# Kernel optimization log

Hardware: AMD Instinct MI355X
Metric: run time of the kernel (lower is better)

Reference implementation:

```python
import jax, jax.numpy as jnp
import numpy as np

D_IN = 2048
D_SAE = 16384
N_RANGES = 4
CTX = 128  # batch == context_length
CHUNK = D_SAE // N_RANGES
LN_EPS = 1e-5


def setup_inputs() -> dict:
    key = jax.random.key(0)
    k1, k2, k3, k4 = jax.random.split(key, 4)
    acts = jax.random.normal(k1, (CTX, D_IN), dtype=jnp.float32)
    # orthogonal-init stand-ins: unit-variance columns
    W_enc_ranges = jax.random.normal(k2, (N_RANGES, D_IN, CHUNK), dtype=jnp.float32) / np.sqrt(D_IN)
    W_dec = jax.random.normal(k3, (D_SAE, D_IN), dtype=jnp.float32) / np.sqrt(D_SAE)
    pos_embeddings = jax.random.normal(k4, (N_RANGES, D_IN), dtype=jnp.float32) * 0.02
    return {
        "acts": acts,
        "W_enc_ranges": W_enc_ranges,
        "b_enc": jnp.zeros((D_SAE,), jnp.float32),
        "b_dec": jnp.zeros((D_IN,), jnp.float32),
        "pos_embeddings": pos_embeddings,
        "ln_weight": jnp.ones((D_SAE,), jnp.float32),
        "ln_bias": jnp.zeros((D_SAE,), jnp.float32),
        "W_dec": W_dec,
    }


def reference(acts, W_enc_ranges, b_enc, b_dec, pos_embeddings, ln_weight, ln_bias, W_dec):
    B, d_in = acts.shape
    n_ranges, _, chunk = W_enc_ranges.shape
    range_size = B // n_ranges  # positions are contiguous blocks per range
    d_sae = n_ranges * chunk

    # gather per position range: [n_ranges, range_size, d_in]
    x = acts.reshape(n_ranges, range_size, d_in)
    x = x + pos_embeddings[:, None, :] - b_dec  # (input + pos_emb) - b_dec

    # per-range GEMM + bias
    pre = jnp.einsum("rbd,rds->rbs", x, W_enc_ranges) + b_enc.reshape(n_ranges, 1, chunk)

    # per-range LayerNorm over the chunk (sliced gamma/beta), biased variance
    mu = jnp.mean(pre, axis=-1, keepdims=True)
    var = jnp.mean(jnp.square(pre - mu), axis=-1, keepdims=True)
    normed = (pre - mu) * jax.lax.rsqrt(var + LN_EPS)
    normed = normed * ln_weight.reshape(n_ranges, 1, chunk) + ln_bias.reshape(n_ranges, 1, chunk)
    feat = jax.nn.relu(normed)  # [n_ranges, range_size, chunk]

    # scatter into block-diagonal encoded [B, d_sae]
    encoded = jnp.zeros((B, d_sae), acts.dtype)
    for r in range(n_ranges):
        encoded = encoded.at[r * range_size:(r + 1) * range_size,
                             r * chunk:(r + 1) * chunk].set(feat[r])

    # decode
    decoded = encoded @ W_dec + b_dec
    return decoded
```

## Files before the change

kernel.cpp:

```cpp
#include <hip/hip_runtime.h>
#include <hip/hip_bf16.h>
#include <stdint.h>


#define D_IN   2048
#define CHUNK  4096
#define RS     32
#define LN_EPS 1e-5f

typedef __attribute__((ext_vector_type(8))) short bf16x8;
typedef __attribute__((ext_vector_type(4))) float f32x4;

#define AS1 __attribute__((address_space(1)))
#define AS3 __attribute__((address_space(3)))

__device__ __forceinline__ void gload_lds16(const float* g, float* l) {
  __builtin_amdgcn_global_load_lds((const AS1 unsigned int*)g,
                                   (AS3 unsigned int*)l, 16, 0, 0);
}

__device__ __forceinline__ unsigned short f2bf(float f) {
  unsigned int u = __float_as_uint(f);
  u += 0x7fffu + ((u >> 16) & 1u);
  return (unsigned short)(u >> 16);
}
__device__ __forceinline__ float bf2f(unsigned short s) {
  return __uint_as_float(((unsigned int)s) << 16);
}

#define MFMA16 __builtin_amdgcn_mfma_f32_16x16x32_bf16

__global__ __launch_bounds__(256) void prep_kernel(
    const float* __restrict__ acts, const float* __restrict__ pos,
    const float* __restrict__ bdec, unsigned short* __restrict__ xfrag) {
  unsigned tid = blockIdx.x * 256u + threadIdx.x;
  unsigned lane = tid & 63u, kt = (tid >> 6) & 63u, mt = (tid >> 12) & 1u, r = tid >> 13;
  unsigned m  = mt * 16 + (lane & 15u);
  unsigned k0 = kt * 32 + (lane >> 4) * 8;
  const float* ap = acts + (size_t)(r * RS + m) * D_IN + k0;
  const float* pp = pos  + (size_t)r * D_IN + k0;
  const float* bp = bdec + k0;
  bf16x8 v;
#pragma unroll
  for (int j = 0; j < 8; ++j) v[j] = (short)f2bf(ap[j] + pp[j] - bp[j]);
  *reinterpret_cast<bf16x8*>(xfrag + (size_t)tid * 8) = v;
}

__global__ __launch_bounds__(256) void enc_kernel(
    const unsigned short* __restrict__ xfrag, const float* __restrict__ Wenc,
    unsigned short* __restrict__ pre_part) {
  const unsigned r = blockIdx.x >> 8, h = (blockIdx.x >> 7) & 1u, nt = blockIdx.x & 127u;
  const unsigned n0 = nt * 32;
  const unsigned w = threadIdx.x >> 6, lane = threadIdx.x & 63u;
  const unsigned col = lane & 15u, g = lane >> 4;

  __shared__ float smem[8192];
  float* mytile = smem + w * 2048;

  const unsigned srow = lane >> 3, scol = (lane & 7u) * 4u;
  const float* gbase = Wenc
      + ((size_t)(r * D_IN + h * 1024 + w * 32 + srow)) * CHUNK + n0 + scol;
  const unsigned short* xa0 = xfrag + ((size_t)(r * 2 + 0) * 64) * 512 + (size_t)lane * 8;
  const unsigned short* xa1 = xfrag + ((size_t)(r * 2 + 1) * 64) * 512 + (size_t)lane * 8;

  f32x4 acc00 = {0.f,0.f,0.f,0.f}, acc01 = acc00, acc10 = acc00, acc11 = acc00;

  auto stageW = [&](unsigned s, unsigned b) {
#pragma unroll
    for (int l = 0; l < 4; ++l) {
      const float* gp = gbase + (size_t)(s * 128 + l * 8) * CHUNK;
      gload_lds16(gp, mytile + b * 1024 + l * 256);
    }
  };

  bf16x8 aC0, aC1, aN0, aN1;
  {
    unsigned kt = h * 32 + w;
    aC0 = *(const bf16x8*)(xa0 + (size_t)kt * 512);
    aC1 = *(const bf16x8*)(xa1 + (size_t)kt * 512);
  }
  stageW(0, 0);

  unsigned buf = 0;
#pragma unroll
  for (int s = 0; s < 8; ++s) {
    if (s < 7) {
      unsigned kt = h * 32 + (s + 1) * 4 + w;
      aN0 = *(const bf16x8*)(xa0 + (size_t)kt * 512);
      aN1 = *(const bf16x8*)(xa1 + (size_t)kt * 512);
      stageW(s + 1, buf ^ 1);
      asm volatile("s_waitcnt vmcnt(6)" ::: "memory");
    } else {
      asm volatile("s_waitcnt vmcnt(0)" ::: "memory");
    }
    const float* tb = mytile + buf * 1024 + g * 8 * 32 + col;
    bf16x8 b0, b1;
#pragma unroll
    for (int j = 0; j < 8; ++j) {
      b0[j] = (short)f2bf(tb[j * 32]);
      b1[j] = (short)f2bf(tb[j * 32 + 16]);
    }
    acc00 = MFMA16(aC0, b0, acc00, 0, 0, 0);
    acc01 = MFMA16(aC0, b1, acc01, 0, 0, 0);
    acc10 = MFMA16(aC1, b0, acc10, 0, 0, 0);
    acc11 = MFMA16(aC1, b1, acc11, 0, 0, 0);
    aC0 = aN0; aC1 = aN1; buf ^= 1;
  }

  __syncthreads();
  float* red = smem;
  if (w > 0) {
#pragma unroll
    for (int i = 0; i < 4; ++i) {
      red[(((w - 1) * 4 + 0) * 64 + lane) * 4 + i] = acc00[i];
      red[(((w - 1) * 4 + 1) * 64 + lane) * 4 + i] = acc01[i];
      red[(((w - 1) * 4 + 2) * 64 + lane) * 4 + i] = acc10[i];
      red[(((w - 1) * 4 + 3) * 64 + lane) * 4 + i] = acc11[i];
    }
  }
  __syncthreads();
  if (w == 0) {
    for (int q = 0; q < 3; ++q)
#pragma unroll
      for (int i = 0; i < 4; ++i) {
        acc00[i] += red[((q * 4 + 0) * 64 + lane) * 4 + i];
        acc01[i] += red[((q * 4 + 1) * 64 + lane) * 4 + i];
        acc10[i] += red[((q * 4 + 2) * 64 + lane) * 4 + i];
        acc11[i] += red[((q * 4 + 3) * 64 + lane) * 4 + i];
      }
    unsigned short* pp = pre_part + (size_t)h * 128 * CHUNK;
#pragma unroll
    for (int i = 0; i < 4; ++i) {
      unsigned row0 = r * RS + g * 4 + i;
      unsigned row1 = row0 + 16;
      pp[(size_t)row0 * CHUNK + n0 + col]      = f2bf(acc00[i]);
      pp[(size_t)row0 * CHUNK + n0 + 16 + col] = f2bf(acc01[i]);
      pp[(size_t)row1 * CHUNK + n0 + col]      = f2bf(acc10[i]);
      pp[(size_t)row1 * CHUNK + n0 + 16 + col] = f2bf(acc11[i]);
    }
  }
}

__global__ __launch_bounds__(256) void lnpack_kernel(
    const unsigned short* __restrict__ pre_part, const float* __restrict__ benc,
    const float* __restrict__ gamma, const float* __restrict__ beta,
    unsigned short* __restrict__ featfrag) {
  const unsigned row = blockIdx.x;
  const unsigned r = row >> 5, m = row & 31u;
  const unsigned t = threadIdx.x;
  const unsigned c0 = t * 16;

  const unsigned short* p0 = pre_part + (size_t)row * CHUNK + c0;
  const unsigned short* p1 = p0 + (size_t)128 * CHUNK;
  const float* bb = benc + (size_t)r * CHUNK + c0;

  bf16x8 u0a = *(const bf16x8*)p0, u0b = *(const bf16x8*)(p0 + 8);
  bf16x8 u1a = *(const bf16x8*)p1, u1b = *(const bf16x8*)(p1 + 8);

  float v[16];
  float s = 0.f, q = 0.f;
#pragma unroll
  for (int j = 0; j < 8; ++j) {
    v[j]     = bf2f((unsigned short)u0a[j]) + bf2f((unsigned short)u1a[j]) + bb[j];
    v[j + 8] = bf2f((unsigned short)u0b[j]) + bf2f((unsigned short)u1b[j]) + bb[j + 8];
  }
#pragma unroll
  for (int j = 0; j < 16; ++j) { s += v[j]; q += v[j] * v[j]; }
#pragma unroll
  for (int off = 1; off < 64; off <<= 1) {
    s += __shfl_xor(s, off, 64);
    q += __shfl_xor(q, off, 64);
  }
  __shared__ float ls[4], lq[4];
  if ((t & 63u) == 0) { ls[t >> 6] = s; lq[t >> 6] = q; }
  __syncthreads();
  s = ls[0] + ls[1] + ls[2] + ls[3];
  q = lq[0] + lq[1] + lq[2] + lq[3];
  float mu  = s * (1.f / CHUNK);
  float var = q * (1.f / CHUNK) - mu * mu;
  float rsd = rsqrtf(var + LN_EPS);

  const float* gp = gamma + (size_t)r * CHUNK + c0;
  const float* bp = beta  + (size_t)r * CHUNK + c0;
  const unsigned mt = m >> 4;
#pragma unroll
  for (int half = 0; half < 2; ++half) {
    bf16x8 o;
#pragma unroll
    for (int j = 0; j < 8; ++j) {
      float x = (v[half * 8 + j] - mu) * rsd * gp[half * 8 + j] + bp[half * 8 + j];
      o[j] = (short)f2bf(fmaxf(x, 0.f));
    }
    unsigned k = c0 + half * 8;
    unsigned kt = k >> 5, grp = (k >> 3) & 3u, ln = (m & 15u) + 16u * grp;
    *(bf16x8*)(featfrag + (((size_t)(r * 2 + mt) * 128 + kt) * 64 + ln) * 8) = o;
  }
}

__global__ __launch_bounds__(256) void dec_kernel(
    const unsigned short* __restrict__ featfrag, const float* __restrict__ Wdec,
    float* __restrict__ part) {
  const unsigned r = blockIdx.x >> 8, h = (blockIdx.x >> 6) & 3u, nt = blockIdx.x & 63u;
  const unsigned n0 = nt * 32;
  const unsigned w = threadIdx.x >> 6, lane = threadIdx.x & 63u;
  const unsigned col = lane & 15u, g = lane >> 4;

  __shared__ float smem[8192];
  float* mytile = smem + w * 2048;

  const unsigned srow = lane >> 3, scol = (lane & 7u) * 4u;
  const float* gbase = Wdec
      + ((size_t)(r * CHUNK + h * 1024 + w * 32 + srow)) * D_IN + n0 + scol;
  const unsigned short* fa0 = featfrag + ((size_t)(r * 2 + 0) * 128) * 512 + (size_t)lane * 8;
  const unsigned short* fa1 = featfrag + ((size_t)(r * 2 + 1) * 128) * 512 + (size_t)lane * 8;

  f32x4 acc00 = {0.f,0.f,0.f,0.f}, acc01 = acc00, acc10 = acc00, acc11 = acc00;

  auto stageW = [&](unsigned s, unsigned b) {
#pragma unroll
    for (int l = 0; l < 4; ++l) {
      const float* gp = gbase + (size_t)(s * 128 + l * 8) * D_IN;
      gload_lds16(gp, mytile + b * 1024 + l * 256);
    }
  };

  bf16x8 aC0, aC1, aN0, aN1;
  {
    unsigned kt = h * 32 + w;
    aC0 = *(const bf16x8*)(fa0 + (size_t)kt * 512);
    aC1 = *(const bf16x8*)(fa1 + (size_t)kt * 512);
  }
  stageW(0, 0);

  unsigned buf = 0;
#pragma unroll
  for (int s = 0; s < 8; ++s) {
    if (s < 7) {
      unsigned kt = h * 32 + (s + 1) * 4 + w;
      aN0 = *(const bf16x8*)(fa0 + (size_t)kt * 512);
      aN1 = *(const bf16x8*)(fa1 + (size_t)kt * 512);
      stageW(s + 1, buf ^ 1);
      asm volatile("s_waitcnt vmcnt(6)" ::: "memory");
    } else {
      asm volatile("s_waitcnt vmcnt(0)" ::: "memory");
    }
    const float* tb = mytile + buf * 1024 + g * 8 * 32 + col;
    bf16x8 b0, b1;
#pragma unroll
    for (int j = 0; j < 8; ++j) {
      b0[j] = (short)f2bf(tb[j * 32]);
      b1[j] = (short)f2bf(tb[j * 32 + 16]);
    }
    acc00 = MFMA16(aC0, b0, acc00, 0, 0, 0);
    acc01 = MFMA16(aC0, b1, acc01, 0, 0, 0);
    acc10 = MFMA16(aC1, b0, acc10, 0, 0, 0);
    acc11 = MFMA16(aC1, b1, acc11, 0, 0, 0);
    aC0 = aN0; aC1 = aN1; buf ^= 1;
  }

  __syncthreads();
  float* red = smem;
  if (w > 0) {
#pragma unroll
    for (int i = 0; i < 4; ++i) {
      red[(((w - 1) * 4 + 0) * 64 + lane) * 4 + i] = acc00[i];
      red[(((w - 1) * 4 + 1) * 64 + lane) * 4 + i] = acc01[i];
      red[(((w - 1) * 4 + 2) * 64 + lane) * 4 + i] = acc10[i];
      red[(((w - 1) * 4 + 3) * 64 + lane) * 4 + i] = acc11[i];
    }
  }
  __syncthreads();
  if (w == 0) {
    for (int q = 0; q < 3; ++q)
#pragma unroll
      for (int i = 0; i < 4; ++i) {
        acc00[i] += red[((q * 4 + 0) * 64 + lane) * 4 + i];
        acc01[i] += red[((q * 4 + 1) * 64 + lane) * 4 + i];
        acc10[i] += red[((q * 4 + 2) * 64 + lane) * 4 + i];
        acc11[i] += red[((q * 4 + 3) * 64 + lane) * 4 + i];
      }
    float* pp = part + (size_t)h * 128 * D_IN;
#pragma unroll
    for (int i = 0; i < 4; ++i) {
      unsigned row0 = r * RS + g * 4 + i;
      unsigned row1 = row0 + 16;
      pp[(size_t)row0 * D_IN + n0 + col]      = acc00[i];
      pp[(size_t)row0 * D_IN + n0 + 16 + col] = acc01[i];
      pp[(size_t)row1 * D_IN + n0 + col]      = acc10[i];
      pp[(size_t)row1 * D_IN + n0 + 16 + col] = acc11[i];
    }
  }
}

__global__ __launch_bounds__(256) void finish_kernel(
    const float* __restrict__ part, const float* __restrict__ bdec,
    float* __restrict__ out) {
  unsigned i = blockIdx.x * 256u + threadIdx.x;
  const size_t stride = (size_t)128 * D_IN / 4;
  f32x4 a0 = ((const f32x4*)part)[i];
  f32x4 a1 = ((const f32x4*)part)[i + stride];
  f32x4 a2 = ((const f32x4*)part)[i + 2 * stride];
  f32x4 a3 = ((const f32x4*)part)[i + 3 * stride];
  f32x4 c  = ((const f32x4*)bdec)[i & 511u];
  f32x4 o;
#pragma unroll
  for (int j = 0; j < 4; ++j) o[j] = ((a0[j] + a1[j]) + (a2[j] + a3[j])) + c[j];
  ((f32x4*)out)[i] = o;
}

extern "C" void kernel_launch(void* const* d_in, const int* in_sizes, int n_in,
                              void* d_out, int out_size, void* d_ws, size_t ws_size,
                              hipStream_t stream) {
  const float* acts = (const float*)d_in[0];
  const float* Wenc = (const float*)d_in[1];
  const float* benc = (const float*)d_in[2];
  const float* bdec = (const float*)d_in[3];
  const float* pos  = (const float*)d_in[4];
  const float* lnw  = (const float*)d_in[5];
  const float* lnb  = (const float*)d_in[6];
  const float* Wdec = (const float*)d_in[7];
  float* out = (float*)d_out;

  char* ws = (char*)d_ws;
  unsigned short* xfrag   = (unsigned short*)ws;
  unsigned short* pre_prt = (unsigned short*)(ws + 512 * 1024);
  unsigned short* featfrg = (unsigned short*)(ws + 2560 * 1024);
  float* part             = (float*)(ws + 3584 * 1024);

  prep_kernel  <<<128,  256, 0, stream>>>(acts, pos, bdec, xfrag);
  enc_kernel   <<<1024, 256, 0, stream>>>(xfrag, Wenc, pre_prt);
  lnpack_kernel<<<128,  256, 0, stream>>>(pre_prt, benc, lnw, lnb, featfrg);
  dec_kernel   <<<1024, 256, 0, stream>>>(featfrg, Wdec, part);
  finish_kernel<<<256,  256, 0, stream>>>(part, bdec, out);
}
```

Measured before the change: 65.77 us.

## Widen GEMM N-tiles, split K across blocks, triple-buffer weight staging

Encoder and decoder GEMM blocks now cover 128 output columns with each wave owning 32 columns, instead of splitting K across waves and reducing through shared memory. K is split across 8 (encoder) or 16 (decoder) blocks, and the partial sums are written in bf16 and summed later in the LN and finish kernels. Weight tiles are loaded into a shared 3-stage ring with block barriers, aiming for wider coalesced global loads and no intra-block reduction. The cost is more partial-sum traffic and lower accuracy from bf16 partials.

```diff
diff --git a/kernel.cpp b/kernel.cpp
--- a/kernel.cpp
+++ b/kernel.cpp
@@ -9,6 +9,7 @@
 #define LN_EPS 1e-5f
 
 typedef __attribute__((ext_vector_type(8))) short bf16x8;
+typedef __attribute__((ext_vector_type(4))) short bf16x4;
 typedef __attribute__((ext_vector_type(4))) float f32x4;
 
 #define AS1 __attribute__((address_space(1)))
@@ -49,95 +50,73 @@
 __global__ __launch_bounds__(256) void enc_kernel(
     const unsigned short* __restrict__ xfrag, const float* __restrict__ Wenc,
     unsigned short* __restrict__ pre_part) {
-  const unsigned r = blockIdx.x >> 8, h = (blockIdx.x >> 7) & 1u, nt = blockIdx.x & 127u;
-  const unsigned n0 = nt * 32;
+  const unsigned r = blockIdx.x >> 8;
+  const unsigned h = (blockIdx.x >> 5) & 7u;
+  const unsigned nt = blockIdx.x & 31u;
+  const unsigned n0 = nt * 128;
   const unsigned w = threadIdx.x >> 6, lane = threadIdx.x & 63u;
   const unsigned col = lane & 15u, g = lane >> 4;
 
-  __shared__ float smem[8192];
-  float* mytile = smem + w * 2048;
-
-  const unsigned srow = lane >> 3, scol = (lane & 7u) * 4u;
-  const float* gbase = Wenc
-      + ((size_t)(r * D_IN + h * 1024 + w * 32 + srow)) * CHUNK + n0 + scol;
+  __shared__ float tiles[3][32 * 128];
+
+  const unsigned srow = w * 8 + (lane >> 5);
+  const unsigned scol = (lane & 31u) * 4u;
+  const float* gbase = Wenc + ((size_t)(r * D_IN + h * 256 + srow)) * CHUNK + n0 + scol;
   const unsigned short* xa0 = xfrag + ((size_t)(r * 2 + 0) * 64) * 512 + (size_t)lane * 8;
   const unsigned short* xa1 = xfrag + ((size_t)(r * 2 + 1) * 64) * 512 + (size_t)lane * 8;
 
   f32x4 acc00 = {0.f,0.f,0.f,0.f}, acc01 = acc00, acc10 = acc00, acc11 = acc00;
 
-  auto stageW = [&](unsigned s, unsigned b) {
+  auto stageW = [&](int s, int b) {
 #pragma unroll
     for (int l = 0; l < 4; ++l) {
-      const float* gp = gbase + (size_t)(s * 128 + l * 8) * CHUNK;
-      gload_lds16(gp, mytile + b * 1024 + l * 256);
-    }
+      const float* gp = gbase + (size_t)(s * 32 + 2 * l) * CHUNK;
+      gload_lds16(gp, &tiles[b][(w * 8 + 2 * l) * 128]);
+    }
+  };
+  auto loadA = [&](int s, bf16x8& A0, bf16x8& A1) {
+    unsigned kt = h * 8 + (unsigned)s;
+    A0 = *(const bf16x8*)(xa0 + (size_t)kt * 512);
+    A1 = *(const bf16x8*)(xa1 + (size_t)kt * 512);
   };
 
   bf16x8 aC0, aC1, aN0, aN1;
-  {
-    unsigned kt = h * 32 + w;
-    aC0 = *(const bf16x8*)(xa0 + (size_t)kt * 512);
-    aC1 = *(const bf16x8*)(xa1 + (size_t)kt * 512);
-  }
   stageW(0, 0);
-
-  unsigned buf = 0;
+  loadA(0, aC0, aC1);
+  stageW(1, 1);
+
 #pragma unroll
   for (int s = 0; s < 8; ++s) {
-    if (s < 7) {
-      unsigned kt = h * 32 + (s + 1) * 4 + w;
-      aN0 = *(const bf16x8*)(xa0 + (size_t)kt * 512);
-      aN1 = *(const bf16x8*)(xa1 + (size_t)kt * 512);
-      stageW(s + 1, buf ^ 1);
-      asm volatile("s_waitcnt vmcnt(6)" ::: "memory");
-    } else {
-      asm volatile("s_waitcnt vmcnt(0)" ::: "memory");
-    }
-    const float* tb = mytile + buf * 1024 + g * 8 * 32 + col;
+    if (s < 7) asm volatile("s_waitcnt vmcnt(4)" ::: "memory");
+    else       asm volatile("s_waitcnt vmcnt(0)" ::: "memory");
+    __builtin_amdgcn_s_barrier();
+    __builtin_amdgcn_sched_barrier(0);
+    if (s < 7) loadA(s + 1, aN0, aN1);
+    if (s < 6) stageW(s + 2, (s + 2) % 3);
+    const float* tb = &tiles[s % 3][(g * 8) * 128 + w * 32 + col];
     bf16x8 b0, b1;
 #pragma unroll
     for (int j = 0; j < 8; ++j) {
-      b0[j] = (short)f2bf(tb[j * 32]);
-      b1[j] = (short)f2bf(tb[j * 32 + 16]);
+      b0[j] = (short)f2bf(tb[j * 128]);
+      b1[j] = (short)f2bf(tb[j * 128 + 16]);
     }
     acc00 = MFMA16(aC0, b0, acc00, 0, 0, 0);
     acc01 = MFMA16(aC0, b1, acc01, 0, 0, 0);
     acc10 = MFMA16(aC1, b0, acc10, 0, 0, 0);
     acc11 = MFMA16(aC1, b1, acc11, 0, 0, 0);
-    aC0 = aN0; aC1 = aN1; buf ^= 1;
-  }
-
-  __syncthreads();
-  float* red = smem;
-  if (w > 0) {
-#pragma unroll
-    for (int i = 0; i < 4; ++i) {
-      red[(((w - 1) * 4 + 0) * 64 + lane) * 4 + i] = acc00[i];
-      red[(((w - 1) * 4 + 1) * 64 + lane) * 4 + i] = acc01[i];
-      red[(((w - 1) * 4 + 2) * 64 + lane) * 4 + i] = acc10[i];
-      red[(((w - 1) * 4 + 3) * 64 + lane) * 4 + i] = acc11[i];
-    }
-  }
-  __syncthreads();
-  if (w == 0) {
-    for (int q = 0; q < 3; ++q)
-#pragma unroll
-      for (int i = 0; i < 4; ++i) {
-        acc00[i] += red[((q * 4 + 0) * 64 + lane) * 4 + i];
-        acc01[i] += red[((q * 4 + 1) * 64 + lane) * 4 + i];
-        acc10[i] += red[((q * 4 + 2) * 64 + lane) * 4 + i];
-        acc11[i] += red[((q * 4 + 3) * 64 + lane) * 4 + i];
-      }
-    unsigned short* pp = pre_part + (size_t)h * 128 * CHUNK;
-#pragma unroll
-    for (int i = 0; i < 4; ++i) {
-      unsigned row0 = r * RS + g * 4 + i;
-      unsigned row1 = row0 + 16;
-      pp[(size_t)row0 * CHUNK + n0 + col]      = f2bf(acc00[i]);
-      pp[(size_t)row0 * CHUNK + n0 + 16 + col] = f2bf(acc01[i]);
-      pp[(size_t)row1 * CHUNK + n0 + col]      = f2bf(acc10[i]);
-      pp[(size_t)row1 * CHUNK + n0 + 16 + col] = f2bf(acc11[i]);
-    }
+    aC0 = aN0; aC1 = aN1;
+  }
+
+  unsigned short* pp = pre_part + (size_t)h * 128 * CHUNK;
+  const unsigned nc = n0 + w * 32 + col;
+#pragma unroll
+  for (int i = 0; i < 4; ++i) {
+    unsigned row0 = r * RS + g * 4 + i;
+    unsigned row1 = row0 + 16;
+    pp[(size_t)row0 * CHUNK + nc]      = f2bf(acc00[i]);
+    pp[(size_t)row0 * CHUNK + nc + 16] = f2bf(acc01[i]);
+    pp[(size_t)row1 * CHUNK + nc]      = f2bf(acc10[i]);
+    pp[(size_t)row1 * CHUNK + nc + 16] = f2bf(acc11[i]);
   }
 }
 
@@ -150,20 +129,21 @@
   const unsigned t = threadIdx.x;
   const unsigned c0 = t * 16;
 
-  const unsigned short* p0 = pre_part + (size_t)row * CHUNK + c0;
-  const unsigned short* p1 = p0 + (size_t)128 * CHUNK;
   const float* bb = benc + (size_t)r * CHUNK + c0;
-
-  bf16x8 u0a = *(const bf16x8*)p0, u0b = *(const bf16x8*)(p0 + 8);
-  bf16x8 u1a = *(const bf16x8*)p1, u1b = *(const bf16x8*)(p1 + 8);
-
   float v[16];
+#pragma unroll
+  for (int j = 0; j < 16; ++j) v[j] = bb[j];
+#pragma unroll
+  for (int hh = 0; hh < 8; ++hh) {
+    const unsigned short* ph = pre_part + ((size_t)hh * 128 + row) * CHUNK + c0;
+    bf16x8 ua = *(const bf16x8*)ph, ub = *(const bf16x8*)(ph + 8);
+#pragma unroll
+    for (int j = 0; j < 8; ++j) {
+      v[j]     += bf2f((unsigned short)ua[j]);
+      v[j + 8] += bf2f((unsigned short)ub[j]);
+    }
+  }
   float s = 0.f, q = 0.f;
-#pragma unroll
-  for (int j = 0; j < 8; ++j) {
-    v[j]     = bf2f((unsigned short)u0a[j]) + bf2f((unsigned short)u1a[j]) + bb[j];
-    v[j + 8] = bf2f((unsigned short)u0b[j]) + bf2f((unsigned short)u1b[j]) + bb[j + 8];
-  }
 #pragma unroll
   for (int j = 0; j < 16; ++j) { s += v[j]; q += v[j] * v[j]; }
 #pragma unroll
@@ -199,112 +179,88 @@
 
 __global__ __launch_bounds__(256) void dec_kernel(
     const unsigned short* __restrict__ featfrag, const float* __restrict__ Wdec,
-    float* __restrict__ part) {
-  const unsigned r = blockIdx.x >> 8, h = (blockIdx.x >> 6) & 3u, nt = blockIdx.x & 63u;
-  const unsigned n0 = nt * 32;
+    unsigned short* __restrict__ part) {
+  const unsigned r = blockIdx.x >> 8;
+  const unsigned h = (blockIdx.x >> 4) & 15u;
+  const unsigned nt = blockIdx.x & 15u;
+  const unsigned n0 = nt * 128;
   const unsigned w = threadIdx.x >> 6, lane = threadIdx.x & 63u;
   const unsigned col = lane & 15u, g = lane >> 4;
 
-  __shared__ float smem[8192];
-  float* mytile = smem + w * 2048;
-
-  const unsigned srow = lane >> 3, scol = (lane & 7u) * 4u;
-  const float* gbase = Wdec
-      + ((size_t)(r * CHUNK + h * 1024 + w * 32 + srow)) * D_IN + n0 + scol;
+  __shared__ float tiles[3][32 * 128];
+
+  const unsigned srow = w * 8 + (lane >> 5);
+  const unsigned scol = (lane & 31u) * 4u;
+  const float* gbase = Wdec + ((size_t)(r * CHUNK + h * 256 + srow)) * D_IN + n0 + scol;
   const unsigned short* fa0 = featfrag + ((size_t)(r * 2 + 0) * 128) * 512 + (size_t)lane * 8;
   const unsigned short* fa1 = featfrag + ((size_t)(r * 2 + 1) * 128) * 512 + (size_t)lane * 8;
 
   f32x4 acc00 = {0.f,0.f,0.f,0.f}, acc01 = acc00, acc10 = acc00, acc11 = acc00;
 
-  auto stageW = [&](unsigned s, unsigned b) {
+  auto stageW = [&](int s, int b) {
 #pragma unroll
     for (int l = 0; l < 4; ++l) {
-      const float* gp = gbase + (size_t)(s * 128 + l * 8) * D_IN;
-      gload_lds16(gp, mytile + b * 1024 + l * 256);
-    }
+      const float* gp = gbase + (size_t)(s * 32 + 2 * l) * D_IN;
+      gload_lds16(gp, &tiles[b][(w * 8 + 2 * l) * 128]);
+    }
+  };
+  auto loadA = [&](int s, bf16x8& A0, bf16x8& A1) {
+    unsigned kt = h * 8 + (unsigned)s;
+    A0 = *(const bf16x8*)(fa0 + (size_t)kt * 512);
+    A1 = *(const bf16x8*)(fa1 + (size_t)kt * 512);
   };
 
   bf16x8 aC0, aC1, aN0, aN1;
-  {
-    unsigned kt = h * 32 + w;
-    aC0 = *(const bf16x8*)(fa0 + (size_t)kt * 512);
-    aC1 = *(const bf16x8*)(fa1 + (size_t)kt * 512);
-  }
   stageW(0, 0);
-
-  unsigned buf = 0;
+  loadA(0, aC0, aC1);
+  stageW(1, 1);
+
 #pragma unroll
   for (int s = 0; s < 8; ++s) {
-    if (s < 7) {
-      unsigned kt = h * 32 + (s + 1) * 4 + w;
-      aN0 = *(const bf16x8*)(fa0 + (size_t)kt * 512);
-      aN1 = *(const bf16x8*)(fa1 + (size_t)kt * 512);
-      stageW(s + 1, buf ^ 1);
-      asm volatile("s_waitcnt vmcnt(6)" ::: "memory");
-    } else {
-      asm volatile("s_waitcnt vmcnt(0)" ::: "memory");
-    }
-    const float* tb = mytile + buf * 1024 + g * 8 * 32 + col;
+    if (s < 7) asm volatile("s_waitcnt vmcnt(4)" ::: "memory");
+    else       asm volatile("s_waitcnt vmcnt(0)" ::: "memory");
+    __builtin_amdgcn_s_barrier();
+    __builtin_amdgcn_sched_barrier(0);
+    if (s < 7) loadA(s + 1, aN0, aN1);
+    if (s < 6) stageW(s + 2, (s + 2) % 3);
+    const float* tb = &tiles[s % 3][(g * 8) * 128 + w * 32 + col];
     bf16x8 b0, b1;
 #pragma unroll
     for (int j = 0; j < 8; ++j) {
-      b0[j] = (short)f2bf(tb[j * 32]);
-      b1[j] = (short)f2bf(tb[j * 32 + 16]);
+      b0[j] = (short)f2bf(tb[j * 128]);
+      b1[j] = (short)f2bf(tb[j * 128 + 16]);
     }
     acc00 = MFMA16(aC0, b0, acc00, 0, 0, 0);
     acc01 = MFMA16(aC0, b1, acc01, 0, 0, 0);
     acc10 = MFMA16(aC1, b0, acc10, 0, 0, 0);
     acc11 = MFMA16(aC1, b1, acc11, 0, 0, 0);
-    aC0 = aN0; aC1 = aN1; buf ^= 1;
-  }
-
-  __syncthreads();
-  float* red = smem;
-  if (w > 0) {
-#pragma unroll
-    for (int i = 0; i < 4; ++i) {
-      red[(((w - 1) * 4 + 0) * 64 + lane) * 4 + i] = acc00[i];
-      red[(((w - 1) * 4 + 1) * 64 + lane) * 4 + i] = acc01[i];
-      red[(((w - 1) * 4 + 2) * 64 + lane) * 4 + i] = acc10[i];
-      red[(((w - 1) * 4 + 3) * 64 + lane) * 4 + i] = acc11[i];
-    }
-  }
-  __syncthreads();
-  if (w == 0) {
-    for (int q = 0; q < 3; ++q)
-#pragma unroll
-      for (int i = 0; i < 4; ++i) {
-        acc00[i] += red[((q * 4 + 0) * 64 + lane) * 4 + i];
-        acc01[i] += red[((q * 4 + 1) * 64 + lane) * 4 + i];
-        acc10[i] += red[((q * 4 + 2) * 64 + lane) * 4 + i];
-        acc11[i] += red[((q * 4 + 3) * 64 + lane) * 4 + i];
-      }
-    float* pp = part + (size_t)h * 128 * D_IN;
-#pragma unroll
-    for (int i = 0; i < 4; ++i) {
-      unsigned row0 = r * RS + g * 4 + i;
-      unsigned row1 = row0 + 16;
-      pp[(size_t)row0 * D_IN + n0 + col]      = acc00[i];
-      pp[(size_t)row0 * D_IN + n0 + 16 + col] = acc01[i];
-      pp[(size_t)row1 * D_IN + n0 + col]      = acc10[i];
-      pp[(size_t)row1 * D_IN + n0 + 16 + col] = acc11[i];
-    }
+    aC0 = aN0; aC1 = aN1;
+  }
+
+  unsigned short* pp = part + (size_t)h * 128 * D_IN;
+  const unsigned nc = n0 + w * 32 + col;
+#pragma unroll
+  for (int i = 0; i < 4; ++i) {
+    unsigned row0 = r * RS + g * 4 + i;
+    unsigned row1 = row0 + 16;
+    pp[(size_t)row0 * D_IN + nc]      = f2bf(acc00[i]);
+    pp[(size_t)row0 * D_IN + nc + 16] = f2bf(acc01[i]);
+    pp[(size_t)row1 * D_IN + nc]      = f2bf(acc10[i]);
+    pp[(size_t)row1 * D_IN + nc + 16] = f2bf(acc11[i]);
   }
 }
 
 __global__ __launch_bounds__(256) void finish_kernel(
-    const float* __restrict__ part, const float* __restrict__ bdec,
+    const unsigned short* __restrict__ part, const float* __restrict__ bdec,
     float* __restrict__ out) {
   unsigned i = blockIdx.x * 256u + threadIdx.x;
-  const size_t stride = (size_t)128 * D_IN / 4;
-  f32x4 a0 = ((const f32x4*)part)[i];
-  f32x4 a1 = ((const f32x4*)part)[i + stride];
-  f32x4 a2 = ((const f32x4*)part)[i + 2 * stride];
-  f32x4 a3 = ((const f32x4*)part)[i + 3 * stride];
-  f32x4 c  = ((const f32x4*)bdec)[i & 511u];
-  f32x4 o;
-#pragma unroll
-  for (int j = 0; j < 4; ++j) o[j] = ((a0[j] + a1[j]) + (a2[j] + a3[j])) + c[j];
+  f32x4 o = ((const f32x4*)bdec)[i & 511u];
+#pragma unroll
+  for (int hh = 0; hh < 16; ++hh) {
+    bf16x4 u = *(const bf16x4*)(part + (size_t)hh * 128 * D_IN + (size_t)i * 4);
+#pragma unroll
+    for (int j = 0; j < 4; ++j) o[j] += bf2f((unsigned short)u[j]);
+  }
   ((f32x4*)out)[i] = o;
 }
 
@@ -324,8 +280,8 @@
   char* ws = (char*)d_ws;
   unsigned short* xfrag   = (unsigned short*)ws;
   unsigned short* pre_prt = (unsigned short*)(ws + 512 * 1024);
-  unsigned short* featfrg = (unsigned short*)(ws + 2560 * 1024);
-  float* part             = (float*)(ws + 3584 * 1024);
+  unsigned short* featfrg = (unsigned short*)(ws + 512 * 1024 + 8*1024*1024);
+  unsigned short* part    = (unsigned short*)(ws + 512 * 1024 + 9*1024*1024);
 
   prep_kernel  <<<128,  256, 0, stream>>>(acts, pos, bdec, xfrag);
   enc_kernel   <<<1024, 256, 0, stream>>>(xfrag, Wenc, pre_prt);
```

Measured after the change: 69.56 us. 5.8% more time.

## Remove split-K partials in encoder and decoder, fuse bias into decoder

Applied to the files above, without the earlier changes.

The encoder no longer splits K into two halves, so each block covers the full 2048 reduction and the LayerNorm kernel reads a single pre-activation buffer instead of summing two partials. The decoder drops its 4-way K split by using 512-thread blocks with 8 waves over the full chunk. It adds b_dec and writes the output directly, which removes the finish kernel and the fp32 partial buffer round-trip. Cost: grid sizes fall to 512 and 256 blocks, so fewer blocks are in flight to stream the weights on a GPU with many CUs, and each block runs a longer serial loop.

```diff
diff --git a/kernel.cpp b/kernel.cpp
--- a/kernel.cpp
+++ b/kernel.cpp
@@ -48,8 +48,8 @@
 
 __global__ __launch_bounds__(256) void enc_kernel(
     const unsigned short* __restrict__ xfrag, const float* __restrict__ Wenc,
-    unsigned short* __restrict__ pre_part) {
-  const unsigned r = blockIdx.x >> 8, h = (blockIdx.x >> 7) & 1u, nt = blockIdx.x & 127u;
+    unsigned short* __restrict__ pre) {
+  const unsigned r = blockIdx.x >> 7, nt = blockIdx.x & 127u;
   const unsigned n0 = nt * 32;
   const unsigned w = threadIdx.x >> 6, lane = threadIdx.x & 63u;
   const unsigned col = lane & 15u, g = lane >> 4;
@@ -59,7 +59,7 @@
 
   const unsigned srow = lane >> 3, scol = (lane & 7u) * 4u;
   const float* gbase = Wenc
-      + ((size_t)(r * D_IN + h * 1024 + w * 32 + srow)) * CHUNK + n0 + scol;
+      + ((size_t)(r * D_IN + w * 32 + srow)) * CHUNK + n0 + scol;
   const unsigned short* xa0 = xfrag + ((size_t)(r * 2 + 0) * 64) * 512 + (size_t)lane * 8;
   const unsigned short* xa1 = xfrag + ((size_t)(r * 2 + 1) * 64) * 512 + (size_t)lane * 8;
 
@@ -75,7 +75,7 @@
 
   bf16x8 aC0, aC1, aN0, aN1;
   {
-    unsigned kt = h * 32 + w;
+    unsigned kt = w;
     aC0 = *(const bf16x8*)(xa0 + (size_t)kt * 512);
     aC1 = *(const bf16x8*)(xa1 + (size_t)kt * 512);
   }
@@ -83,9 +83,9 @@
 
   unsigned buf = 0;
 #pragma unroll
-  for (int s = 0; s < 8; ++s) {
-    if (s < 7) {
-      unsigned kt = h * 32 + (s + 1) * 4 + w;
+  for (int s = 0; s < 16; ++s) {
+    if (s < 15) {
+      unsigned kt = (s + 1) * 4 + w;
       aN0 = *(const bf16x8*)(xa0 + (size_t)kt * 512);
       aN1 = *(const bf16x8*)(xa1 + (size_t)kt * 512);
       stageW(s + 1, buf ^ 1);
@@ -128,21 +128,20 @@
         acc10[i] += red[((q * 4 + 2) * 64 + lane) * 4 + i];
         acc11[i] += red[((q * 4 + 3) * 64 + lane) * 4 + i];
       }
-    unsigned short* pp = pre_part + (size_t)h * 128 * CHUNK;
 #pragma unroll
     for (int i = 0; i < 4; ++i) {
       unsigned row0 = r * RS + g * 4 + i;
       unsigned row1 = row0 + 16;
-      pp[(size_t)row0 * CHUNK + n0 + col]      = f2bf(acc00[i]);
-      pp[(size_t)row0 * CHUNK + n0 + 16 + col] = f2bf(acc01[i]);
-      pp[(size_t)row1 * CHUNK + n0 + col]      = f2bf(acc10[i]);
-      pp[(size_t)row1 * CHUNK + n0 + 16 + col] = f2bf(acc11[i]);
+      pre[(size_t)row0 * CHUNK + n0 + col]      = f2bf(acc00[i]);
+      pre[(size_t)row0 * CHUNK + n0 + 16 + col] = f2bf(acc01[i]);
+      pre[(size_t)row1 * CHUNK + n0 + col]      = f2bf(acc10[i]);
+      pre[(size_t)row1 * CHUNK + n0 + 16 + col] = f2bf(acc11[i]);
     }
   }
 }
 
 __global__ __launch_bounds__(256) void lnpack_kernel(
-    const unsigned short* __restrict__ pre_part, const float* __restrict__ benc,
+    const unsigned short* __restrict__ pre, const float* __restrict__ benc,
     const float* __restrict__ gamma, const float* __restrict__ beta,
     unsigned short* __restrict__ featfrag) {
   const unsigned row = blockIdx.x;
@@ -150,19 +149,17 @@
   const unsigned t = threadIdx.x;
   const unsigned c0 = t * 16;
 
-  const unsigned short* p0 = pre_part + (size_t)row * CHUNK + c0;
-  const unsigned short* p1 = p0 + (size_t)128 * CHUNK;
+  const unsigned short* p0 = pre + (size_t)row * CHUNK + c0;
   const float* bb = benc + (size_t)r * CHUNK + c0;
 
-  bf16x8 u0a = *(const bf16x8*)p0, u0b = *(const bf16x8*)(p0 + 8);
-  bf16x8 u1a = *(const bf16x8*)p1, u1b = *(const bf16x8*)(p1 + 8);
+  bf16x8 ua = *(const bf16x8*)p0, ub = *(const bf16x8*)(p0 + 8);
 
   float v[16];
   float s = 0.f, q = 0.f;
 #pragma unroll
   for (int j = 0; j < 8; ++j) {
-    v[j]     = bf2f((unsigned short)u0a[j]) + bf2f((unsigned short)u1a[j]) + bb[j];
-    v[j + 8] = bf2f((unsigned short)u0b[j]) + bf2f((unsigned short)u1b[j]) + bb[j + 8];
+    v[j]     = bf2f((unsigned short)ua[j]) + bb[j];
+    v[j + 8] = bf2f((unsigned short)ub[j]) + bb[j + 8];
   }
 #pragma unroll
   for (int j = 0; j < 16; ++j) { s += v[j]; q += v[j] * v[j]; }
@@ -197,20 +194,20 @@
   }
 }
 
-__global__ __launch_bounds__(256) void dec_kernel(
+__global__ __launch_bounds__(512) void dec_kernel(
     const unsigned short* __restrict__ featfrag, const float* __restrict__ Wdec,
-    float* __restrict__ part) {
-  const unsigned r = blockIdx.x >> 8, h = (blockIdx.x >> 6) & 3u, nt = blockIdx.x & 63u;
+    const float* __restrict__ bdec, float* __restrict__ out) {
+  const unsigned r = blockIdx.x >> 6, nt = blockIdx.x & 63u;
   const unsigned n0 = nt * 32;
   const unsigned w = threadIdx.x >> 6, lane = threadIdx.x & 63u;
   const unsigned col = lane & 15u, g = lane >> 4;
 
-  __shared__ float smem[8192];
+  __shared__ float smem[16384];
   float* mytile = smem + w * 2048;
 
   const unsigned srow = lane >> 3, scol = (lane & 7u) * 4u;
   const float* gbase = Wdec
-      + ((size_t)(r * CHUNK + h * 1024 + w * 32 + srow)) * D_IN + n0 + scol;
+      + ((size_t)(r * CHUNK + w * 32 + srow)) * D_IN + n0 + scol;
   const unsigned short* fa0 = featfrag + ((size_t)(r * 2 + 0) * 128) * 512 + (size_t)lane * 8;
   const unsigned short* fa1 = featfrag + ((size_t)(r * 2 + 1) * 128) * 512 + (size_t)lane * 8;
 
@@ -219,14 +216,14 @@
   auto stageW = [&](unsigned s, unsigned b) {
 #pragma unroll
     for (int l = 0; l < 4; ++l) {
-      const float* gp = gbase + (size_t)(s * 128 + l * 8) * D_IN;
+      const float* gp = gbase + (size_t)(s * 256 + l * 8) * D_IN;
       gload_lds16(gp, mytile + b * 1024 + l * 256);
     }
   };
 
   bf16x8 aC0, aC1, aN0, aN1;
   {
-    unsigned kt = h * 32 + w;
+    unsigned kt = w;
     aC0 = *(const bf16x8*)(fa0 + (size_t)kt * 512);
     aC1 = *(const bf16x8*)(fa1 + (size_t)kt * 512);
   }
@@ -234,9 +231,9 @@
 
   unsigned buf = 0;
 #pragma unroll
-  for (int s = 0; s < 8; ++s) {
-    if (s < 7) {
-      unsigned kt = h * 32 + (s + 1) * 4 + w;
+  for (int s = 0; s < 16; ++s) {
+    if (s < 15) {
+      unsigned kt = (s + 1) * 8 + w;
       aN0 = *(const bf16x8*)(fa0 + (size_t)kt * 512);
       aN1 = *(const bf16x8*)(fa1 + (size_t)kt * 512);
       stageW(s + 1, buf ^ 1);
@@ -271,7 +268,7 @@
   }
   __syncthreads();
   if (w == 0) {
-    for (int q = 0; q < 3; ++q)
+    for (int q = 0; q < 7; ++q)
 #pragma unroll
       for (int i = 0; i < 4; ++i) {
         acc00[i] += red[((q * 4 + 0) * 64 + lane) * 4 + i];
@@ -279,33 +276,17 @@
         acc10[i] += red[((q * 4 + 2) * 64 + lane) * 4 + i];
         acc11[i] += red[((q * 4 + 3) * 64 + lane) * 4 + i];
       }
-    float* pp = part + (size_t)h * 128 * D_IN;
+    float b0 = bdec[n0 + col], b1 = bdec[n0 + 16 + col];
 #pragma unroll
     for (int i = 0; i < 4; ++i) {
       unsigned row0 = r * RS + g * 4 + i;
       unsigned row1 = row0 + 16;
-      pp[(size_t)row0 * D_IN + n0 + col]      = acc00[i];
-      pp[(size_t)row0 * D_IN + n0 + 16 + col] = acc01[i];
-      pp[(size_t)row1 * D_IN + n0 + col]      = acc10[i];
-      pp[(size_t)row1 * D_IN + n0 + 16 + col] = acc11[i];
-    }
-  }
-}
-
-__global__ __launch_bounds__(256) void finish_kernel(
-    const float* __restrict__ part, const float* __restrict__ bdec,
-    float* __restrict__ out) {
-  unsigned i = blockIdx.x * 256u + threadIdx.x;
-  const size_t stride = (size_t)128 * D_IN / 4;
-  f32x4 a0 = ((const f32x4*)part)[i];
-  f32x4 a1 = ((const f32x4*)part)[i + stride];
-  f32x4 a2 = ((const f32x4*)part)[i + 2 * stride];
-  f32x4 a3 = ((const f32x4*)part)[i + 3 * stride];
-  f32x4 c  = ((const f32x4*)bdec)[i & 511u];
-  f32x4 o;
-#pragma unroll
-  for (int j = 0; j < 4; ++j) o[j] = ((a0[j] + a1[j]) + (a2[j] + a3[j])) + c[j];
-  ((f32x4*)out)[i] = o;
+      out[(size_t)row0 * D_IN + n0 + col]      = acc00[i] + b0;
+      out[(size_t)row0 * D_IN + n0 + 16 + col] = acc01[i] + b1;
+      out[(size_t)row1 * D_IN + n0 + col]      = acc10[i] + b0;
+      out[(size_t)row1 * D_IN + n0 + 16 + col] = acc11[i] + b1;
+    }
+  }
 }
 
 extern "C" void kernel_launch(void* const* d_in, const int* in_sizes, int n_in,
@@ -323,13 +304,11 @@
 
   char* ws = (char*)d_ws;
   unsigned short* xfrag   = (unsigned short*)ws;
-  unsigned short* pre_prt = (unsigned short*)(ws + 512 * 1024);
-  unsigned short* featfrg = (unsigned short*)(ws + 2560 * 1024);
-  float* part             = (float*)(ws + 3584 * 1024);
-
-  prep_kernel  <<<128,  256, 0, stream>>>(acts, pos, bdec, xfrag);
-  enc_kernel   <<<1024, 256, 0, stream>>>(xfrag, Wenc, pre_prt);
-  lnpack_kernel<<<128,  256, 0, stream>>>(pre_prt, benc, lnw, lnb, featfrg);
-  dec_kernel   <<<1024, 256, 0, stream>>>(featfrg, Wdec, part);
-  finish_kernel<<<256,  256, 0, stream>>>(part, bdec, out);
-}
+  unsigned short* pre     = (unsigned short*)(ws + 512 * 1024);
+  unsigned short* featfrg = (unsigned short*)(ws + 1536 * 1024);
+
+  prep_kernel  <<<128, 256, 0, stream>>>(acts, pos, bdec, xfrag);
+  enc_kernel   <<<512, 256, 0, stream>>>(xfrag, Wenc, pre);
+  lnpack_kernel<<<128, 256, 0, stream>>>(pre, benc, lnw, lnb, featfrg);
+  dec_kernel   <<<256, 512, 0, stream>>>(featfrg, Wdec, bdec, out);
+}
```

Result: faster. 61.38 us (-6.7%).
